# Kernel tuning notes

Measured on AMD Instinct MI355X. Metric: run time of the kernel, lower is better.

The kernel has to match this reference:

```python
import jax, jax.numpy as jnp
import numpy as np

N_HEAD = 16
HEAD_DIM = 64
R_VALUE = 256
EPS_LN = 1e-5


def _orf(x, omega, b):
    # orthogonal random features: sqrt(2/r) * cos(x @ omega.T + b)
    r = b.shape[0]
    return jnp.sqrt(2.0 / r) * jnp.cos(x @ omega.T + b)


def _layernorm(x, gamma, beta):
    m = jnp.mean(x, axis=-1, keepdims=True)
    v = jnp.var(x, axis=-1, keepdims=True)
    return (x - m) / jnp.sqrt(v + EPS_LN) * gamma + beta


def setup_inputs() -> dict:
    key = jax.random.key(0)
    ks = jax.random.split(key, 12)
    B, L = 4, 2048
    dm = N_HEAD * HEAD_DIM  # 1024
    inp = {}
    inp["pre_query"] = jax.random.normal(ks[0], (B, L, dm), jnp.float32)
    inp["pre_key"] = jax.random.normal(ks[1], (B, L, dm), jnp.float32)
    inp["pre_value"] = jax.random.normal(ks[2], (B, L, dm), jnp.float32)
    inp["wq"] = jax.random.normal(ks[3], (dm, dm), jnp.float32) * 0.02
    inp["wk"] = jax.random.normal(ks[4], (dm, dm), jnp.float32) * 0.02
    inp["wv"] = jax.random.normal(ks[5], (dm, dm), jnp.float32) * 0.02
    inp["wo"] = jax.random.normal(ks[6], (dm, dm), jnp.float32) * 0.02
    inp["gamma"] = jnp.ones((dm,), jnp.float32)
    inp["beta"] = jnp.zeros((dm,), jnp.float32)
    G = jax.random.normal(ks[7], (R_VALUE, HEAD_DIM), jnp.float32)
    omega, _ = jnp.linalg.qr(G)  # (r, head_dim), orthonormal columns
    inp["omega"] = omega
    inp["b"] = jax.random.uniform(ks[8], (R_VALUE,), jnp.float32) * 2.0 * jnp.pi
    return inp


def reference(pre_query, pre_key, pre_value, wq, wk, wv, wo, gamma, beta, omega, b):
    B, L, dm = pre_query.shape
    H, D = N_HEAD, dm // N_HEAD
    q = (pre_query @ wq.T).reshape(B, L, H, D)
    k = (pre_key @ wk.T).reshape(B, L, H, D)
    v = (pre_value @ wv.T).reshape(B, L, H, D)

    qp = _orf(q, omega, b)  # (B,L,H,R)
    kp = _orf(k, omega, b)  # (B,L,H,R)

    # causal Performer attention as a linear-attention recurrence:
    # S_t = S_{t-1} + k'_t v_t^T ; z_t = z_{t-1} + k'_t
    # out_t = (q'_t . S_t) / clamp(q'_t . z_t)
    R = b.shape[0]
    S0 = jnp.zeros((B, H, R, D), qp.dtype)
    z0 = jnp.zeros((B, H, R), qp.dtype)

    def step(carry, xs):
        S, z = carry
        q_t, k_t, v_t = xs  # (B,H,R),(B,H,R),(B,H,D)
        S = S + k_t[..., :, None] * v_t[..., None, :]
        z = z + k_t
        num = jnp.einsum('bhr,bhrd->bhd', q_t, S)
        den = jnp.clip(jnp.einsum('bhr,bhr->bh', q_t, z), 1e-6, None)
        return (S, z), num / (den[..., None] + 1e-6)

    xs = (qp.transpose(1, 0, 2, 3), kp.transpose(1, 0, 2, 3), v.transpose(1, 0, 2, 3))
    _, out = jax.lax.scan(step, (S0, z0), xs)  # (L,B,H,D)
    out = out.transpose(1, 0, 2, 3).reshape(B, L, dm)

    pre_result = out @ wo.T
    return _layernorm(pre_result + pre_query, gamma, beta)
```

## Files before the change

kernel.cpp:

```cpp
#include <hip/hip_runtime.h>
#include <hip/hip_bf16.h>


typedef float f4 __attribute__((ext_vector_type(4)));
typedef __attribute__((ext_vector_type(8))) short bf16x8;
typedef __attribute__((ext_vector_type(4))) float f32x4;
typedef unsigned short u16x4 __attribute__((ext_vector_type(4)));
typedef unsigned short u16x8 __attribute__((ext_vector_type(8)));

#define B_  4
#define L_  2048
#define H_  16
#define D_  64
#define DM_ 1024
#define R_  256
#define C_  64
#define NC_ (L_ / C_)
#define M_  (B_ * L_)
#define M2_ (M_ * H_)

static __device__ __forceinline__ unsigned short f2bu(float x) {
    __hip_bfloat16 h = __float2bfloat16(x);
    return *(unsigned short*)&h;
}
static __device__ __forceinline__ float bu2f(unsigned short u) {
    union { unsigned int i; float f; } c; c.i = ((unsigned int)u) << 16; return c.f;
}

typedef __attribute__((address_space(3))) void lds_void_t;
typedef __attribute__((address_space(1))) const void gvoid_t;
static __device__ __forceinline__ void gload16(const void* g, void* l) {
    __builtin_amdgcn_global_load_lds((gvoid_t*)g, (lds_void_t*)l, 16, 0, 0);
}

__launch_bounds__(256)
__global__ void cvt_bf16(const float* __restrict__ in, unsigned short* __restrict__ out, int n4) {
    int i = blockIdx.x * 256 + threadIdx.x;
    if (i < n4) {
        f4 v = *(const f4*)&in[(size_t)i * 4];
        ushort4 o;
        o.x = f2bu(v[0]); o.y = f2bu(v[1]); o.z = f2bu(v[2]); o.w = f2bu(v[3]);
        *(ushort4*)&out[(size_t)i * 4] = o;
    }
}

__launch_bounds__(256)
__global__ void cvt_bf16_x3(const float* __restrict__ i0, const float* __restrict__ i1,
                            const float* __restrict__ i2,
                            unsigned short* __restrict__ o0, unsigned short* __restrict__ o1,
                            unsigned short* __restrict__ o2, int n4) {
    const int z = blockIdx.z;
    const float* in = (z == 0) ? i0 : (z == 1) ? i1 : i2;
    unsigned short* out = (z == 0) ? o0 : (z == 1) ? o1 : o2;
    int i = blockIdx.x * 256 + threadIdx.x;
    if (i < n4) {
        f4 v = *(const f4*)&in[(size_t)i * 4];
        ushort4 o;
        o.x = f2bu(v[0]); o.y = f2bu(v[1]); o.z = f2bu(v[2]); o.w = f2bu(v[3]);
        *(ushort4*)&out[(size_t)i * 4] = o;
    }
}

__launch_bounds__(256)
__global__ void gemm_mfma_b3(const unsigned short* __restrict__ A0, const unsigned short* __restrict__ A1,
                             const unsigned short* __restrict__ A2,
                             const unsigned short* __restrict__ B0, const unsigned short* __restrict__ B1,
                             const unsigned short* __restrict__ B2,
                             unsigned short* __restrict__ C0, unsigned short* __restrict__ C1,
                             unsigned short* __restrict__ C2,
                             int M, int N, int K) {
    __shared__ unsigned short Asl[2][128 * 32];
    __shared__ unsigned short Bsl[2][128 * 32];
    const int z = blockIdx.z;
    const unsigned short* A  = (z == 0) ? A0 : (z == 1) ? A1 : A2;
    const unsigned short* Bw = (z == 0) ? B0 : (z == 1) ? B1 : B2;
    unsigned short*       Cb = (z == 0) ? C0 : (z == 1) ? C1 : C2;
    const int t = threadIdx.x;
    const int lane = t & 63, w = t >> 6;
    const int wr = w >> 1, wc = w & 1;
    const int nwg = gridDim.x * gridDim.y;
    const int bid = blockIdx.y * gridDim.x + blockIdx.x;
    const int cpx = nwg >> 3;
    const int swz = (bid & 7) * cpx + (bid >> 3);
    const int row0 = (swz / gridDim.x) * 128, col0 = (swz % gridDim.x) * 128;
    const int sr0 = t >> 2, sk0 = (t & 3) * 8;
    const int lg = lane >> 4, lr = lane & 15;

#define STAGE_B3(buf, kkk) do { \
        gload16(&A [(size_t)(row0 + sr0)      * K + (kkk) + sk0], &Asl[buf][t * 8]); \
        gload16(&A [(size_t)(row0 + sr0 + 64) * K + (kkk) + sk0], &Asl[buf][(t + 256) * 8]); \
        gload16(&Bw[(size_t)(col0 + sr0)      * K + (kkk) + sk0], &Bsl[buf][t * 8]); \
        gload16(&Bw[(size_t)(col0 + sr0 + 64) * K + (kkk) + sk0], &Bsl[buf][(t + 256) * 8]); \
    } while (0)

    f32x4 acc[4][4] = {};
    STAGE_B3(0, 0);
    __syncthreads();
    int cur = 0;
    for (int kk = 0; kk < K; kk += 32) {
        if (kk + 32 < K) STAGE_B3(cur ^ 1, kk + 32);
        bf16x8 af[4], bfr[4];
#pragma unroll
        for (int m = 0; m < 4; ++m)
            af[m] = *(const bf16x8*)&Asl[cur][(wr * 64 + m * 16 + lr) * 32 + lg * 8];
#pragma unroll
        for (int n = 0; n < 4; ++n)
            bfr[n] = *(const bf16x8*)&Bsl[cur][(wc * 64 + n * 16 + lr) * 32 + lg * 8];
#pragma unroll
        for (int m = 0; m < 4; ++m)
#pragma unroll
            for (int n = 0; n < 4; ++n)
                acc[m][n] = __builtin_amdgcn_mfma_f32_16x16x32_bf16(af[m], bfr[n], acc[m][n], 0, 0, 0);
        __syncthreads();
        cur ^= 1;
    }
#undef STAGE_B3
#pragma unroll
    for (int m = 0; m < 4; ++m)
#pragma unroll
        for (int n = 0; n < 4; ++n)
#pragma unroll
            for (int i = 0; i < 4; ++i) {
                int r  = row0 + wr * 64 + m * 16 + lg * 4 + i;
                int cc = col0 + wc * 64 + n * 16 + lr;
                Cb[(size_t)r * N + cc] = f2bu(acc[m][n][i]);
            }
}

__launch_bounds__(256)
__global__ void gemm_out(const unsigned short* __restrict__ A,
                         const unsigned short* __restrict__ Bw,
                         const float* __restrict__ resid,
                         float* __restrict__ Cf,
                         int M, int N, int K) {
    __shared__ unsigned short Asl[2][64 * 32];
    __shared__ unsigned short Bsl[2][128 * 32];
    const int t = threadIdx.x;
    const int lane = t & 63, w = t >> 6;
    const int nwg = gridDim.x * gridDim.y;
    const int bid = blockIdx.y * gridDim.x + blockIdx.x;
    const int cpx = nwg >> 3;
    const int swz = (bid & 7) * cpx + (bid >> 3);
    const int row0 = (swz / gridDim.x) * 64, col0 = (swz % gridDim.x) * 128;
    const int sr0 = t >> 2, sk0 = (t & 3) * 8;
    const int lg = lane >> 4, lr = lane & 15;

#define STAGE_O(buf, kkk) do { \
        gload16(&A [(size_t)(row0 + sr0)      * K + (kkk) + sk0], &Asl[buf][t * 8]); \
        gload16(&Bw[(size_t)(col0 + sr0)      * K + (kkk) + sk0], &Bsl[buf][t * 8]); \
        gload16(&Bw[(size_t)(col0 + sr0 + 64) * K + (kkk) + sk0], &Bsl[buf][(t + 256) * 8]); \
    } while (0)

    f32x4 acc[4][2] = {};
    STAGE_O(0, 0);
    __syncthreads();
    int cur = 0;
    for (int kk = 0; kk < K; kk += 32) {
        if (kk + 32 < K) STAGE_O(cur ^ 1, kk + 32);
        bf16x8 af[4], bfr[2];
#pragma unroll
        for (int m = 0; m < 4; ++m)
            af[m] = *(const bf16x8*)&Asl[cur][(m * 16 + lr) * 32 + lg * 8];
#pragma unroll
        for (int n = 0; n < 2; ++n)
            bfr[n] = *(const bf16x8*)&Bsl[cur][(w * 32 + n * 16 + lr) * 32 + lg * 8];
#pragma unroll
        for (int m = 0; m < 4; ++m)
#pragma unroll
            for (int n = 0; n < 2; ++n)
                acc[m][n] = __builtin_amdgcn_mfma_f32_16x16x32_bf16(af[m], bfr[n], acc[m][n], 0, 0, 0);
        __syncthreads();
        cur ^= 1;
    }
#undef STAGE_O
#pragma unroll
    for (int m = 0; m < 4; ++m)
#pragma unroll
        for (int n = 0; n < 2; ++n)
#pragma unroll
            for (int i = 0; i < 4; ++i) {
                int r  = row0 + m * 16 + lg * 4 + i;
                int cc = col0 + w * 32 + n * 16 + lr;
                size_t off = (size_t)r * N + cc;
                Cf[off] = acc[m][n][i] + resid[off];
            }
}

#define RS_STRIDE 272
__launch_bounds__(256)
__global__ void feat_mfma_b2(const unsigned short* __restrict__ X0, const unsigned short* __restrict__ X1,
                             const unsigned short* __restrict__ om,
                             const float* __restrict__ bvec,
                             unsigned short* __restrict__ O0, unsigned short* __restrict__ O1) {
    __shared__ unsigned short Xs[2 * 64 * 32];
    __shared__ unsigned short Pool[64 * RS_STRIDE];
    const int z = blockIdx.z;
    const unsigned short* X = z ? X1 : X0;
    unsigned short* out = z ? O1 : O0;
    const int t = threadIdx.x;
    const int lane = t & 63, w = t >> 6;
    const int lg = lane >> 4, lr = lane & 15;
    const int m0 = blockIdx.x * 64;

#pragma unroll
    for (int i = 0; i < 2; ++i) {
        int cch = i * 256 + t;
        int ks = cch >> 8, row = (cch >> 2) & 63, sub = cch & 3;
        gload16(&X[(size_t)(m0 + row) * 64 + ks * 32 + sub * 8], &Xs[cch * 8]);
    }
#pragma unroll
    for (int i = 0; i < 8; ++i) {
        int cch = i * 256 + t;
        int ks = cch >> 10, r = (cch >> 2) & 255, sub = cch & 3;
        gload16(&om[(size_t)r * 64 + ks * 32 + sub * 8], &Pool[cch * 8]);
    }
    __syncthreads();

    f32x4 acc[4][4] = {};
#pragma unroll
    for (int ks = 0; ks < 2; ++ks) {
        bf16x8 af[4], bfr[4];
#pragma unroll
        for (int m = 0; m < 4; ++m)
            af[m] = *(const bf16x8*)&Xs[ks * 2048 + (m * 16 + lr) * 32 + lg * 8];
#pragma unroll
        for (int n = 0; n < 4; ++n)
            bfr[n] = *(const bf16x8*)&Pool[ks * 8192 + (w * 64 + n * 16 + lr) * 32 + lg * 8];
#pragma unroll
        for (int m = 0; m < 4; ++m)
#pragma unroll
            for (int n = 0; n < 4; ++n)
                acc[m][n] = __builtin_amdgcn_mfma_f32_16x16x32_bf16(af[m], bfr[n], acc[m][n], 0, 0, 0);
    }
    __syncthreads();

    const float scale = 0.08838834764831845f;
#pragma unroll
    for (int n = 0; n < 4; ++n) {
        const int col = w * 64 + n * 16 + lr;
        const float bb = bvec[col];
#pragma unroll
        for (int m = 0; m < 4; ++m)
#pragma unroll
            for (int ii = 0; ii < 4; ++ii)
                Pool[(m * 16 + lg * 4 + ii) * RS_STRIDE + col] = f2bu(scale * __cosf(acc[m][n][ii] + bb));
    }
    __syncthreads();
#pragma unroll
    for (int i = 0; i < 8; ++i) {
        int cch = i * 256 + t;
        int row = cch >> 5, colc = (cch & 31) * 8;
        u16x8 vv = *(const u16x8*)&Pool[row * RS_STRIDE + colc];
        *(u16x8*)&out[(size_t)(m0 + row) * 256 + colc] = vv;
    }
}

__launch_bounds__(256)
__global__ void passA_mfma(const unsigned short* __restrict__ kp, const unsigned short* __restrict__ vb,
                           unsigned short* __restrict__ kvT, float* __restrict__ ksum) {
    __shared__ __align__(16) unsigned short KPt[256][72];
    __shared__ __align__(16) unsigned short Vt[64][72];
    const int c = blockIdx.x, h = blockIdx.y, bz = blockIdx.z;
    const int t = threadIdx.x;
    const int lane = t & 63, w = t >> 6;
    const int lg = lane >> 4, lr = lane & 15;
    const int l0 = c * C_;
    const int bh = bz * H_ + h;

    {
        const int l4 = (t & 15) * 4, rs = (t >> 4) * 16;
        u16x8 row[4][2];
#pragma unroll
        for (int i = 0; i < 4; ++i) {
            const unsigned short* src = &kp[((size_t)(bz * L_ + l0 + l4 + i) * H_ + h) * R_ + rs];
            row[i][0] = *(const u16x8*)src;
            row[i][1] = *(const u16x8*)(src + 8);
        }
#pragma unroll
        for (int q = 0; q < 16; ++q) {
            u16x4 pk = { row[0][q >> 3][q & 7], row[1][q >> 3][q & 7],
                         row[2][q >> 3][q & 7], row[3][q >> 3][q & 7] };
            *(u16x4*)&KPt[rs + q][l4] = pk;
        }
    }
    {
        const int d4 = (t & 15) * 4, ls = (t >> 4) * 4;
        u16x4 x[4];
#pragma unroll
        for (int i = 0; i < 4; ++i)
            x[i] = *(const u16x4*)&vb[(size_t)(bz * L_ + l0 + ls + i) * DM_ + h * 64 + d4];
#pragma unroll
        for (int q = 0; q < 4; ++q) {
            u16x4 pk = { x[0][q], x[1][q], x[2][q], x[3][q] };
            *(u16x4*)&Vt[d4 + q][ls] = pk;
        }
    }
    __syncthreads();

    f32x4 acc[4][4] = {};
#pragma unroll
    for (int ks = 0; ks < 2; ++ks) {
        bf16x8 af[4], bfr[4];
#pragma unroll
        for (int m = 0; m < 4; ++m)
            af[m] = *(const bf16x8*)&KPt[64 * w + 16 * m + lr][ks * 32 + lg * 8];
#pragma unroll
        for (int n = 0; n < 4; ++n)
            bfr[n] = *(const bf16x8*)&Vt[16 * n + lr][ks * 32 + lg * 8];
#pragma unroll
        for (int m = 0; m < 4; ++m)
#pragma unroll
            for (int n = 0; n < 4; ++n)
                acc[m][n] = __builtin_amdgcn_mfma_f32_16x16x32_bf16(af[m], bfr[n], acc[m][n], 0, 0, 0);
    }
    size_t sbase = ((size_t)(bh * NC_ + c)) * 64 * R_;
#pragma unroll
    for (int n = 0; n < 4; ++n)
#pragma unroll
        for (int m = 0; m < 4; ++m) {
            int d = 16 * n + lr;
            int r = 64 * w + 16 * m + lg * 4;
            u16x4 pk = { f2bu(acc[m][n][0]), f2bu(acc[m][n][1]),
                         f2bu(acc[m][n][2]), f2bu(acc[m][n][3]) };
            *(u16x4*)&kvT[sbase + (size_t)d * R_ + r] = pk;
        }
    {
        float s = 0.f;
#pragma unroll
        for (int j = 0; j < 8; ++j) {
            u16x8 vv = *(const u16x8*)&KPt[t][j * 8];
#pragma unroll
            for (int q = 0; q < 8; ++q) s += bu2f(vv[q]);
        }
        ksum[((size_t)(bh * NC_ + c)) * R_ + t] = s;
    }
}

__launch_bounds__(256)
__global__ void passB_chain(unsigned short* __restrict__ kvT, float* __restrict__ ksum) {
    const int d = blockIdx.x, h = blockIdx.y, bz = blockIdx.z;
    const int t = threadIdx.x;
    const int bh = bz * H_ + h;
    size_t base = ((size_t)bh * NC_ * 64 + d) * R_ + t;
    const size_t cstride = (size_t)64 * R_;
    float run = 0.f;
    for (int c = 0; c < NC_; ++c) {
        size_t idx = base + (size_t)c * cstride;
        float tmp = bu2f(kvT[idx]);
        kvT[idx] = f2bu(run);
        run += tmp;
    }
    if (d == 0) {
        float rz = 0.f;
        for (int c = 0; c < NC_; ++c) {
            size_t idx = ((size_t)bh * NC_ + c) * R_ + t;
            float tmp = ksum[idx];
            ksum[idx] = rz;
            rz += tmp;
        }
    }
}

__launch_bounds__(256)
__global__ void passC_mfma(const unsigned short* __restrict__ qp, const unsigned short* __restrict__ kp,
                           const unsigned short* __restrict__ vb, const unsigned short* __restrict__ kvT,
                           const float* __restrict__ zpref, unsigned short* __restrict__ attnb) {
    __shared__ __align__(16) unsigned short Sl[64 * 256];
    __shared__ __align__(16) unsigned short Vt[80][72];
    __shared__ __align__(16) unsigned short As[64][72];

    const int c = blockIdx.x, h = blockIdx.y, bz = blockIdx.z;
    const int t = threadIdx.x;
    const int lane = t & 63, w = t >> 6;
    const int lg = lane >> 4, lr = lane & 15;
    const int l0 = c * C_;
    const int bh = bz * H_ + h;
    const size_t sbase = ((size_t)(bh * NC_ + c)) * 64 * R_;
    const size_t zbase = ((size_t)(bh * NC_ + c)) * R_;

#pragma unroll
    for (int i = 0; i < 8; ++i) {
        int idx = i * 256 + t;
        int row = idx >> 5, s = idx & 31;
        gload16(&kvT[sbase + (size_t)row * R_ + ((s ^ (row & 7)) << 3)], &Sl[idx * 8]);
    }

    {
        const int d4 = (t & 15) * 4, ls = (t >> 4) * 4;
        u16x4 x[4];
#pragma unroll
        for (int i = 0; i < 4; ++i)
            x[i] = *(const u16x4*)&vb[(size_t)(bz * L_ + l0 + ls + i) * DM_ + h * 64 + d4];
#pragma unroll
        for (int q = 0; q < 4; ++q) {
            u16x4 pk = { x[0][q], x[1][q], x[2][q], x[3][q] };
            *(u16x4*)&Vt[d4 + q][ls] = pk;
        }
    }
    if (t < 16) {
        u16x4 ones = { 0x3F80, 0x3F80, 0x3F80, 0x3F80 };
        *(u16x4*)&Vt[64][t * 4] = ones;
    }

    const size_t qrow = ((size_t)(bz * L_ + l0 + 16 * w + lr) * H_ + h) * R_;
    bf16x8 aq[8];
#pragma unroll
    for (int ks = 0; ks < 8; ++ks) aq[ks] = *(const bf16x8*)&qp[qrow + ks * 32 + lg * 8];

    f32x4 sacc[4] = {};
#pragma unroll
    for (int half = 0; half < 2; ++half) {
        bf16x8 bk[4][4];
#pragma unroll
        for (int k2 = 0; k2 < 4; ++k2)
#pragma unroll
            for (int n = 0; n < 4; ++n)
                bk[k2][n] = *(const bf16x8*)&kp[((size_t)(bz * L_ + l0 + 16 * n + lr) * H_ + h) * R_
                                                + (half * 4 + k2) * 32 + lg * 8];
        __builtin_amdgcn_s_setprio(1);
#pragma unroll
        for (int k2 = 0; k2 < 4; ++k2)
#pragma unroll
            for (int n = 0; n < 4; ++n)
                sacc[n] = __builtin_amdgcn_mfma_f32_16x16x32_bf16(aq[half * 4 + k2], bk[k2][n], sacc[n], 0, 0, 0);
        __builtin_amdgcn_s_setprio(0);
    }
#pragma unroll
    for (int n = 0; n < 4; ++n)
#pragma unroll
        for (int ii = 0; ii < 4; ++ii) {
            int i_loc = 16 * w + lg * 4 + ii;
            int j_loc = 16 * n + lr;
            As[i_loc][j_loc] = (j_loc <= i_loc) ? f2bu(sacc[n][ii]) : (unsigned short)0;
        }

    u16x8 zu[8];
#pragma unroll
    for (int ks = 0; ks < 8; ++ks) {
        f4 z0 = *(const f4*)&zpref[zbase + ks * 32 + lg * 8];
        f4 z1 = *(const f4*)&zpref[zbase + ks * 32 + lg * 8 + 4];
        zu[ks] = u16x8{ f2bu(z0[0]), f2bu(z0[1]), f2bu(z0[2]), f2bu(z0[3]),
                        f2bu(z1[0]), f2bu(z1[1]), f2bu(z1[2]), f2bu(z1[3]) };
    }
    __syncthreads();

    f32x4 oacc[4] = {};
    f32x4 dacc = {};
    __builtin_amdgcn_s_setprio(1);
#pragma unroll
    for (int ks = 0; ks < 8; ++ks) {
#pragma unroll
        for (int n = 0; n < 4; ++n) {
            int row = 16 * n + lr;
            int slot = (ks * 4 + lg) ^ (lr & 7);
            bf16x8 bs = *(const bf16x8*)&Sl[row * 256 + slot * 8];
            oacc[n] = __builtin_amdgcn_mfma_f32_16x16x32_bf16(aq[ks], bs, oacc[n], 0, 0, 0);
        }
        dacc = __builtin_amdgcn_mfma_f32_16x16x32_bf16(aq[ks], *(bf16x8*)&zu[ks], dacc, 0, 0, 0);
    }

    f32x4 racc = {};
#pragma unroll
    for (int ks = 0; ks < 2; ++ks) {
        bf16x8 aa = *(const bf16x8*)&As[16 * w + lr][ks * 32 + lg * 8];
#pragma unroll
        for (int n = 0; n < 4; ++n) {
            bf16x8 bv = *(const bf16x8*)&Vt[16 * n + lr][ks * 32 + lg * 8];
            oacc[n] = __builtin_amdgcn_mfma_f32_16x16x32_bf16(aa, bv, oacc[n], 0, 0, 0);
        }
        bf16x8 b4 = *(const bf16x8*)&Vt[64 + lr][ks * 32 + lg * 8];
        racc = __builtin_amdgcn_mfma_f32_16x16x32_bf16(aa, b4, racc, 0, 0, 0);
    }
    __builtin_amdgcn_s_setprio(0);

#pragma unroll
    for (int ii = 0; ii < 4; ++ii) {
        float rs_ = __shfl(racc[ii], lane & 48, 64);
        float den = rs_ + dacc[ii];
        float inv = 1.f / (fmaxf(den, 1e-6f) + 1e-6f);
#pragma unroll
        for (int n = 0; n < 4; ++n)
            attnb[(size_t)(bz * L_ + l0 + 16 * w + lg * 4 + ii) * DM_ + h * 64 + 16 * n + lr] =
                f2bu(oacc[n][ii] * inv);
    }
}

__launch_bounds__(256)
__global__ void ln_kernel(float* __restrict__ io, const float* __restrict__ gamma,
                          const float* __restrict__ beta) {
    __shared__ float wsum[4], wsum2[4];
    const int row = blockIdx.x;
    const int t = threadIdx.x;
    f4 x = *(const f4*)&io[(size_t)row * DM_ + t * 4];
    float s  = x[0] + x[1] + x[2] + x[3];
    float s2 = x[0]*x[0] + x[1]*x[1] + x[2]*x[2] + x[3]*x[3];
#pragma unroll
    for (int o = 32; o > 0; o >>= 1) {
        s  += __shfl_down(s, o);
        s2 += __shfl_down(s2, o);
    }
    if ((t & 63) == 0) { wsum[t >> 6] = s; wsum2[t >> 6] = s2; }
    __syncthreads();
    s  = wsum[0]  + wsum[1]  + wsum[2]  + wsum[3];
    s2 = wsum2[0] + wsum2[1] + wsum2[2] + wsum2[3];
    const float m = s * (1.f / DM_);
    const float var = s2 * (1.f / DM_) - m * m;
    const float rstd = rsqrtf(var + 1e-5f);
    f4 g  = *(const f4*)&gamma[t * 4];
    f4 bb = *(const f4*)&beta[t * 4];
    f4 o = (x - m) * rstd * g + bb;
    *(f4*)&io[(size_t)row * DM_ + t * 4] = o;
}

extern "C" void kernel_launch(void* const* d_in, const int* in_sizes, int n_in,
                              void* d_out, int out_size, void* d_ws, size_t ws_size,
                              hipStream_t stream) {
    const float* pre_q = (const float*)d_in[0];
    const float* pre_k = (const float*)d_in[1];
    const float* pre_v = (const float*)d_in[2];
    const float* wq    = (const float*)d_in[3];
    const float* wk    = (const float*)d_in[4];
    const float* wv    = (const float*)d_in[5];
    const float* wo    = (const float*)d_in[6];
    const float* gamma = (const float*)d_in[7];
    const float* beta  = (const float*)d_in[8];
    const float* omega = (const float*)d_in[9];
    const float* bvec  = (const float*)d_in[10];

    const size_t NEED = 226ull << 20;
    if (ws_size < NEED) return;

    char* w = (char*)d_ws;
    unsigned short* qp    = (unsigned short*)(w);
    unsigned short* kp    = (unsigned short*)(w + (64ull << 20));
    unsigned short* kvT   = (unsigned short*)(w + (128ull << 20));
    unsigned short* vb    = (unsigned short*)(w + (192ull << 20));
    unsigned short* attnb = (unsigned short*)(w + (208ull << 20));
    float*          ksum  = (float*)(w + (224ull << 20));
    unsigned short* aq    = (unsigned short*)(w);
    unsigned short* ak    = (unsigned short*)(w + (16ull << 20));
    unsigned short* av    = (unsigned short*)(w + (32ull << 20));
    unsigned short* wq_bf = (unsigned short*)(w + (48ull << 20));
    unsigned short* wk_bf = (unsigned short*)(w + (50ull << 20));
    unsigned short* wv_bf = (unsigned short*)(w + (52ull << 20));
    unsigned short* qx    = (unsigned short*)(w + (128ull << 20));
    unsigned short* kx    = (unsigned short*)(w + (144ull << 20));
    unsigned short* om_bf = (unsigned short*)(w + (208ull << 20));
    unsigned short* wo_bf = (unsigned short*)(w + (64ull << 20));
    float*          outb  = (float*)d_out;

    const int n4_big = M_ * DM_ / 4;
    const int n4_w   = DM_ * DM_ / 4;
    const int n4_om  = R_ * D_ / 4;
    dim3 gg3(DM_ / 128, M_ / 128, 3);
    dim3 ggo(DM_ / 128, M_ / 64);

    cvt_bf16_x3<<<dim3((n4_big + 255) / 256, 1, 3), 256, 0, stream>>>(
        pre_q, pre_k, pre_v, aq, ak, av, n4_big);
    cvt_bf16_x3<<<dim3((n4_w + 255) / 256, 1, 3), 256, 0, stream>>>(
        wq, wk, wv, wq_bf, wk_bf, wv_bf, n4_w);
    cvt_bf16<<<(n4_om + 255) / 256, 256, 0, stream>>>(omega, om_bf, n4_om);

    gemm_mfma_b3<<<gg3, 256, 0, stream>>>(aq, ak, av, wq_bf, wk_bf, wv_bf,
                                          qx, kx, vb, M_, DM_, DM_);
    feat_mfma_b2<<<dim3(M2_ / 64, 1, 2), 256, 0, stream>>>(qx, kx, om_bf, bvec, qp, kp);

    passA_mfma<<<dim3(NC_, H_, B_), 256, 0, stream>>>(kp, vb, kvT, ksum);
    passB_chain<<<dim3(64, H_, B_), 256, 0, stream>>>(kvT, ksum);
    passC_mfma<<<dim3(NC_, H_, B_), 256, 0, stream>>>(qp, kp, vb, kvT, ksum, attnb);

    cvt_bf16<<<(n4_w + 255) / 256, 256, 0, stream>>>(wo, wo_bf, n4_w);
    gemm_out<<<ggo, 256, 0, stream>>>(attnb, wo_bf, pre_q, outb, M_, DM_, DM_);
    ln_kernel<<<M_, 256, 0, stream>>>(outb, gamma, beta);
}
```

Baseline: 302.4 us.

## Swizzle LDS tiles, load GEMM B fragments directly to registers, vectorize prefix scan

```diff
diff --git a/kernel.cpp b/kernel.cpp
--- a/kernel.cpp
+++ b/kernel.cpp
@@ -70,7 +70,6 @@
                              unsigned short* __restrict__ C2,
                              int M, int N, int K) {
     __shared__ unsigned short Asl[2][128 * 32];
-    __shared__ unsigned short Bsl[2][128 * 32];
     const int z = blockIdx.z;
     const unsigned short* A  = (z == 0) ? A0 : (z == 1) ? A1 : A2;
     const unsigned short* Bw = (z == 0) ? B0 : (z == 1) ? B1 : B2;
@@ -83,38 +82,48 @@
     const int cpx = nwg >> 3;
     const int swz = (bid & 7) * cpx + (bid >> 3);
     const int row0 = (swz / gridDim.x) * 128, col0 = (swz % gridDim.x) * 128;
-    const int sr0 = t >> 2, sk0 = (t & 3) * 8;
+    const int sr0 = t >> 2;
+    const int ssw = (((t & 3) ^ ((t >> 3) & 3)) * 8);
     const int lg = lane >> 4, lr = lane & 15;
-
-#define STAGE_B3(buf, kkk) do { \
-        gload16(&A [(size_t)(row0 + sr0)      * K + (kkk) + sk0], &Asl[buf][t * 8]); \
-        gload16(&A [(size_t)(row0 + sr0 + 64) * K + (kkk) + sk0], &Asl[buf][(t + 256) * 8]); \
-        gload16(&Bw[(size_t)(col0 + sr0)      * K + (kkk) + sk0], &Bsl[buf][t * 8]); \
-        gload16(&Bw[(size_t)(col0 + sr0 + 64) * K + (kkk) + sk0], &Bsl[buf][(t + 256) * 8]); \
+    const int aslot = (lg ^ ((lr >> 1) & 3)) * 8;
+
+#define STAGE_A(buf, kkk) do { \
+        gload16(&A[(size_t)(row0 + sr0)      * K + (kkk) + ssw], &Asl[buf][t * 8]); \
+        gload16(&A[(size_t)(row0 + sr0 + 64) * K + (kkk) + ssw], &Asl[buf][(t + 256) * 8]); \
     } while (0)
+#define LOADB(dst, kkk) do { \
+        _Pragma("unroll") \
+        for (int n = 0; n < 4; ++n) \
+            dst[n] = *(const bf16x8*)&Bw[(size_t)(col0 + wc * 64 + n * 16 + lr) * K + (kkk) + lg * 8]; \
+    } while (0)
 
     f32x4 acc[4][4] = {};
-    STAGE_B3(0, 0);
+    bf16x8 bcur[4], bnxt[4];
+    STAGE_A(0, 0);
+    LOADB(bcur, 0);
     __syncthreads();
     int cur = 0;
     for (int kk = 0; kk < K; kk += 32) {
-        if (kk + 32 < K) STAGE_B3(cur ^ 1, kk + 32);
-        bf16x8 af[4], bfr[4];
-#pragma unroll
-        for (int m = 0; m < 4; ++m)
-            af[m] = *(const bf16x8*)&Asl[cur][(wr * 64 + m * 16 + lr) * 32 + lg * 8];
-#pragma unroll
-        for (int n = 0; n < 4; ++n)
-            bfr[n] = *(const bf16x8*)&Bsl[cur][(wc * 64 + n * 16 + lr) * 32 + lg * 8];
+        if (kk + 32 < K) {
+            STAGE_A(cur ^ 1, kk + 32);
+            LOADB(bnxt, kk + 32);
+        }
+        bf16x8 af[4];
+#pragma unroll
+        for (int m = 0; m < 4; ++m)
+            af[m] = *(const bf16x8*)&Asl[cur][(wr * 64 + m * 16 + lr) * 32 + aslot];
 #pragma unroll
         for (int m = 0; m < 4; ++m)
 #pragma unroll
             for (int n = 0; n < 4; ++n)
-                acc[m][n] = __builtin_amdgcn_mfma_f32_16x16x32_bf16(af[m], bfr[n], acc[m][n], 0, 0, 0);
+                acc[m][n] = __builtin_amdgcn_mfma_f32_16x16x32_bf16(af[m], bcur[n], acc[m][n], 0, 0, 0);
         __syncthreads();
+#pragma unroll
+        for (int n = 0; n < 4; ++n) bcur[n] = bnxt[n];
         cur ^= 1;
     }
-#undef STAGE_B3
+#undef STAGE_A
+#undef LOADB
 #pragma unroll
     for (int m = 0; m < 4; ++m)
 #pragma unroll
@@ -134,7 +143,6 @@
                          float* __restrict__ Cf,
                          int M, int N, int K) {
     __shared__ unsigned short Asl[2][64 * 32];
-    __shared__ unsigned short Bsl[2][128 * 32];
     const int t = threadIdx.x;
     const int lane = t & 63, w = t >> 6;
     const int nwg = gridDim.x * gridDim.y;
@@ -142,37 +150,46 @@
     const int cpx = nwg >> 3;
     const int swz = (bid & 7) * cpx + (bid >> 3);
     const int row0 = (swz / gridDim.x) * 64, col0 = (swz % gridDim.x) * 128;
-    const int sr0 = t >> 2, sk0 = (t & 3) * 8;
+    const int sr0 = t >> 2;
+    const int ssw = (((t & 3) ^ ((t >> 3) & 3)) * 8);
     const int lg = lane >> 4, lr = lane & 15;
-
-#define STAGE_O(buf, kkk) do { \
-        gload16(&A [(size_t)(row0 + sr0)      * K + (kkk) + sk0], &Asl[buf][t * 8]); \
-        gload16(&Bw[(size_t)(col0 + sr0)      * K + (kkk) + sk0], &Bsl[buf][t * 8]); \
-        gload16(&Bw[(size_t)(col0 + sr0 + 64) * K + (kkk) + sk0], &Bsl[buf][(t + 256) * 8]); \
+    const int aslot = (lg ^ ((lr >> 1) & 3)) * 8;
+
+#define STAGE_O(buf, kkk) \
+        gload16(&A[(size_t)(row0 + sr0) * K + (kkk) + ssw], &Asl[buf][t * 8])
+#define LOADB_O(dst, kkk) do { \
+        _Pragma("unroll") \
+        for (int n = 0; n < 2; ++n) \
+            dst[n] = *(const bf16x8*)&Bw[(size_t)(col0 + w * 32 + n * 16 + lr) * K + (kkk) + lg * 8]; \
     } while (0)
 
     f32x4 acc[4][2] = {};
+    bf16x8 bcur[2], bnxt[2];
     STAGE_O(0, 0);
+    LOADB_O(bcur, 0);
     __syncthreads();
     int cur = 0;
     for (int kk = 0; kk < K; kk += 32) {
-        if (kk + 32 < K) STAGE_O(cur ^ 1, kk + 32);
-        bf16x8 af[4], bfr[2];
-#pragma unroll
-        for (int m = 0; m < 4; ++m)
-            af[m] = *(const bf16x8*)&Asl[cur][(m * 16 + lr) * 32 + lg * 8];
-#pragma unroll
-        for (int n = 0; n < 2; ++n)
-            bfr[n] = *(const bf16x8*)&Bsl[cur][(w * 32 + n * 16 + lr) * 32 + lg * 8];
+        if (kk + 32 < K) {
+            STAGE_O(cur ^ 1, kk + 32);
+            LOADB_O(bnxt, kk + 32);
+        }
+        bf16x8 af[4];
+#pragma unroll
+        for (int m = 0; m < 4; ++m)
+            af[m] = *(const bf16x8*)&Asl[cur][(m * 16 + lr) * 32 + aslot];
 #pragma unroll
         for (int m = 0; m < 4; ++m)
 #pragma unroll
             for (int n = 0; n < 2; ++n)
-                acc[m][n] = __builtin_amdgcn_mfma_f32_16x16x32_bf16(af[m], bfr[n], acc[m][n], 0, 0, 0);
+                acc[m][n] = __builtin_amdgcn_mfma_f32_16x16x32_bf16(af[m], bcur[n], acc[m][n], 0, 0, 0);
         __syncthreads();
+#pragma unroll
+        for (int n = 0; n < 2; ++n) bcur[n] = bnxt[n];
         cur ^= 1;
     }
 #undef STAGE_O
+#undef LOADB_O
 #pragma unroll
     for (int m = 0; m < 4; ++m)
 #pragma unroll
@@ -201,18 +218,21 @@
     const int lane = t & 63, w = t >> 6;
     const int lg = lane >> 4, lr = lane & 15;
     const int m0 = blockIdx.x * 64;
+    const int aslot = (lg ^ ((lr >> 1) & 3)) * 8;
 
 #pragma unroll
     for (int i = 0; i < 2; ++i) {
         int cch = i * 256 + t;
-        int ks = cch >> 8, row = (cch >> 2) & 63, sub = cch & 3;
-        gload16(&X[(size_t)(m0 + row) * 64 + ks * 32 + sub * 8], &Xs[cch * 8]);
+        int ks = cch >> 8, row = (cch >> 2) & 63;
+        int sub = ((cch & 3) ^ ((cch >> 3) & 3)) * 8;
+        gload16(&X[(size_t)(m0 + row) * 64 + ks * 32 + sub], &Xs[cch * 8]);
     }
 #pragma unroll
     for (int i = 0; i < 8; ++i) {
         int cch = i * 256 + t;
-        int ks = cch >> 10, r = (cch >> 2) & 255, sub = cch & 3;
-        gload16(&om[(size_t)r * 64 + ks * 32 + sub * 8], &Pool[cch * 8]);
+        int ks = cch >> 10, r = (cch >> 2) & 255;
+        int sub = ((cch & 3) ^ ((cch >> 3) & 3)) * 8;
+        gload16(&om[(size_t)r * 64 + ks * 32 + sub], &Pool[cch * 8]);
     }
     __syncthreads();
 
@@ -222,10 +242,10 @@
         bf16x8 af[4], bfr[4];
 #pragma unroll
         for (int m = 0; m < 4; ++m)
-            af[m] = *(const bf16x8*)&Xs[ks * 2048 + (m * 16 + lr) * 32 + lg * 8];
+            af[m] = *(const bf16x8*)&Xs[ks * 2048 + (m * 16 + lr) * 32 + aslot];
 #pragma unroll
         for (int n = 0; n < 4; ++n)
-            bfr[n] = *(const bf16x8*)&Pool[ks * 8192 + (w * 64 + n * 16 + lr) * 32 + lg * 8];
+            bfr[n] = *(const bf16x8*)&Pool[ks * 8192 + (w * 64 + n * 16 + lr) * 32 + aslot];
 #pragma unroll
         for (int m = 0; m < 4; ++m)
 #pragma unroll
@@ -338,24 +358,29 @@
 
 __launch_bounds__(256)
 __global__ void passB_chain(unsigned short* __restrict__ kvT, float* __restrict__ ksum) {
-    const int d = blockIdx.x, h = blockIdx.y, bz = blockIdx.z;
+    const int bx = blockIdx.x, h = blockIdx.y, bz = blockIdx.z;
     const int t = threadIdx.x;
     const int bh = bz * H_ + h;
-    size_t base = ((size_t)bh * NC_ * 64 + d) * R_ + t;
+    const int idx = bx * 256 + t;
+    const int d = idx >> 6;
+    const int rg = (idx & 63) * 4;
+    size_t base = ((size_t)bh * NC_ * 64 + d) * R_ + rg;
     const size_t cstride = (size_t)64 * R_;
-    float run = 0.f;
+    float run0 = 0.f, run1 = 0.f, run2 = 0.f, run3 = 0.f;
     for (int c = 0; c < NC_; ++c) {
-        size_t idx = base + (size_t)c * cstride;
-        float tmp = bu2f(kvT[idx]);
-        kvT[idx] = f2bu(run);
-        run += tmp;
-    }
-    if (d == 0) {
+        size_t ix = base + (size_t)c * cstride;
+        u16x4 v = *(const u16x4*)&kvT[ix];
+        u16x4 o = { f2bu(run0), f2bu(run1), f2bu(run2), f2bu(run3) };
+        *(u16x4*)&kvT[ix] = o;
+        run0 += bu2f(v[0]); run1 += bu2f(v[1]);
+        run2 += bu2f(v[2]); run3 += bu2f(v[3]);
+    }
+    if (bx == 0) {
         float rz = 0.f;
         for (int c = 0; c < NC_; ++c) {
-            size_t idx = ((size_t)bh * NC_ + c) * R_ + t;
-            float tmp = ksum[idx];
-            ksum[idx] = rz;
+            size_t ix = ((size_t)bh * NC_ + c) * R_ + t;
+            float tmp = ksum[ix];
+            ksum[ix] = rz;
             rz += tmp;
         }
     }
@@ -566,7 +591,7 @@
     feat_mfma_b2<<<dim3(M2_ / 64, 1, 2), 256, 0, stream>>>(qx, kx, om_bf, bvec, qp, kp);
 
     passA_mfma<<<dim3(NC_, H_, B_), 256, 0, stream>>>(kp, vb, kvT, ksum);
-    passB_chain<<<dim3(64, H_, B_), 256, 0, stream>>>(kvT, ksum);
+    passB_chain<<<dim3(16, H_, B_), 256, 0, stream>>>(kvT, ksum);
     passC_mfma<<<dim3(NC_, H_, B_), 256, 0, stream>>>(qp, kp, vb, kvT, ksum, attnb);
 
     cvt_bf16<<<(n4_w + 255) / 256, 256, 0, stream>>>(wo, wo_bf, n4_w);
```

Result: slower. 358.4 us (+18.5%).
